# Performance work log

Measured on AMD Instinct MI355X. Metric: run time of the kernel, lower is better.

The kernel has to match this reference:

```python
import jax, jax.numpy as jnp
import numpy as np

B, S, K = 32, 256, 3   # batch, lattice length, max predecessors
D = 512                # dim_embedding == dim_rnn_input
H = 512                # dim_hidden
V = 50257              # vocab_size
L = 128                # label_vocab_size


def lattice_lstm(x, prev_idx, prev_w, Wih, Whh, bih, bhh):
    # x: [B,S,D]; prev_idx/prev_w: [B,S,K]; PyTorch LSTM gate layout (i,f,g,o).
    Bs, Sl, _ = x.shape
    Hh = Whh.shape[1]
    b_ar = jnp.arange(Bs)[:, None]  # [B,1] batch index for gather

    def step(carry, xs):
        hs, cs = carry              # stored per-timestep states [S,B,H]
        t, x_t, idx_t, w_t = xs     # [], [B,D], [B,K], [B,K]
        # weighted gather-pool over lattice predecessors; hs/cs are zero-init
        # so at t==0 this yields the zero initial state, as in the original.
        h = jnp.einsum('bk,bkh->bh', w_t, hs[idx_t, b_ar])
        c = jnp.einsum('bk,bkh->bh', w_t, cs[idx_t, b_ar])
        gates = x_t @ Wih.T + h @ Whh.T + (bih + bhh)  # [B,4H]
        i, f, g, o = jnp.split(gates, 4, axis=-1)
        c_new = jax.nn.sigmoid(f) * c + jax.nn.sigmoid(i) * jnp.tanh(g)
        h_new = jax.nn.sigmoid(o) * jnp.tanh(c_new)
        return (hs.at[t].set(h_new), cs.at[t].set(c_new)), h_new

    z = jnp.zeros((Sl, Bs, Hh), x.dtype)
    xs = (jnp.arange(Sl), x.swapaxes(0, 1), prev_idx.swapaxes(0, 1), prev_w.swapaxes(0, 1))
    _, outs = jax.lax.scan(step, (z, z), xs)
    return outs.swapaxes(0, 1)  # [B,S,H]


def _forward(inputs, positions, prev_idx, prev_w, emb, Wih, Whh, bih, bhh, W_lin, b_lin):
    x = emb[inputs]  # [B,S,D]
    out = lattice_lstm(x, prev_idx, prev_w, Wih, Whh, bih, bhh)
    # max-pool over the [start, end) span per batch element
    t_idx = jnp.arange(out.shape[1])[None, :]
    start, end = positions[:, 0:1], positions[:, 1:2]
    mask = (t_idx >= start) & (t_idx < end)                  # [B,S]
    pooled = jnp.where(mask[..., None], out, -1e30).max(axis=1)
    pooled = jnp.where(end > start, pooled, 0.0)             # empty span -> zeros
    return pooled @ W_lin.T + b_lin                          # [B,L]


def setup_inputs():
    key = jax.random.key(0)
    ks = jax.random.split(key, 12)
    inputs = jax.random.randint(ks[0], (B, S), 0, V)
    positions = jnp.concatenate([
        jax.random.randint(ks[1], (B, 1), 0, S // 2),
        jax.random.randint(ks[2], (B, 1), S // 2, S + 1)], axis=1)
    # predecessor indices must point strictly before t (DAG topological order)
    t = jnp.arange(S)[None, :, None]
    prev_idx = jax.random.randint(ks[3], (B, S, K), 0, S) % jnp.maximum(t, 1)
    u = jax.random.uniform(ks[4], (B, S, K)) + 0.1
    prev_w = u / u.sum(-1, keepdims=True)  # lattice marginals, sum to 1
    s = 1.0 / np.sqrt(H)
    emb = jax.random.uniform(ks[5], (V, D), minval=-0.1, maxval=0.1)
    Wih = jax.random.uniform(ks[6], (4 * H, D), minval=-s, maxval=s)
    Whh = jax.random.uniform(ks[7], (4 * H, H), minval=-s, maxval=s)
    bih = jax.random.uniform(ks[8], (4 * H,), minval=-s, maxval=s)
    bhh = jax.random.uniform(ks[9], (4 * H,), minval=-s, maxval=s)
    W_lin = jax.random.uniform(ks[10], (L, H), minval=-s, maxval=s)
    b_lin = jax.random.uniform(ks[11], (L,), minval=-s, maxval=s)
    return {"inputs": inputs, "positions": positions, "prev_idx": prev_idx,
            "prev_w": prev_w, "emb": emb, "Wih": Wih, "Whh": Whh,
            "bih": bih, "bhh": bhh, "W_lin": W_lin, "b_lin": b_lin}


def reference(inputs, positions, prev_idx, prev_w, emb, Wih, Whh, bih, bhh, W_lin, b_lin):
    return _forward(inputs, positions, prev_idx, prev_w, emb, Wih, Whh, bih, bhh, W_lin, b_lin)
```

## Files before the change

### kernel.cpp

```cpp
#include <hip/hip_runtime.h>


#define BB 32
#define SS 256
#define KKK 3
#define DD 512
#define HH 512
#define G4 2048
#define LL 128
#define NG 2
#define GS 8
#define NB 16
#define HSL 64

typedef __attribute__((ext_vector_type(4))) float f32x4;
typedef __attribute__((ext_vector_type(8))) short bf16x8;

__device__ __forceinline__ float blo(unsigned u){ return __builtin_bit_cast(float, u << 16); }
__device__ __forceinline__ float bhi(unsigned u){ return __builtin_bit_cast(float, u & 0xffff0000u); }
__device__ __forceinline__ unsigned f2bf(float f){
  unsigned x = __builtin_bit_cast(unsigned, f);
  x = x + 0x7fffu + ((x >> 16) & 1u);
  return x >> 16;
}
__device__ __forceinline__ float sigm(float x){ return 1.0f / (1.0f + __expf(-x)); }
__device__ __forceinline__ float tanh_(float x){
  float ax = fabsf(x);
  float e = __expf(-2.0f * ax);
  float r = (1.0f - e) / (1.0f + e);
  return x < 0.0f ? -r : r;
}
__device__ __forceinline__ void glds16(const void* g, void* lds){
  __builtin_amdgcn_global_load_lds((const __attribute__((address_space(1))) unsigned int*)g,
                                   (__attribute__((address_space(3))) unsigned int*)lds, 16, 0, 0);
}

__global__ __launch_bounds__(256) void prep_kernel(
    const int* __restrict__ inputs, const float* __restrict__ emb,
    const float* __restrict__ Wih, const float* __restrict__ bih, const float* __restrict__ bhh,
    unsigned short* __restrict__ Xb, unsigned short* __restrict__ Wihb, float* __restrict__ bias)
{
  int blk = blockIdx.x, tid = threadIdx.x;
  if (blk < 512){
    int row = blk * 16 + (tid >> 4);
    int d0 = (tid & 15) * 32;
    int b = row & 31, t = row >> 5;
    int tok = inputs[b * SS + t];
    const float* src = emb + (size_t)tok * DD + d0;
    unsigned short* dst = Xb + (size_t)row * DD + d0;
    #pragma unroll
    for (int j = 0; j < 32; j += 4){
      float4 v = *(const float4*)(src + j);
      uint2 o;
      o.x = f2bf(v.x) | (f2bf(v.y) << 16);
      o.y = f2bf(v.z) | (f2bf(v.w) << 16);
      *(uint2*)(dst + j) = o;
    }
  } else if (blk < 640){
    int row = (blk - 512) * 16 + (tid >> 4);
    int d0 = (tid & 15) * 32;
    const float* src = Wih + (size_t)row * DD + d0;
    unsigned short* dst = Wihb + (size_t)row * DD + d0;
    #pragma unroll
    for (int j = 0; j < 32; j += 4){
      float4 v = *(const float4*)(src + j);
      uint2 o;
      o.x = f2bf(v.x) | (f2bf(v.y) << 16);
      o.y = f2bf(v.z) | (f2bf(v.w) << 16);
      *(uint2*)(dst + j) = o;
    }
  } else {
    for (int n = tid; n < G4; n += 256) bias[n] = bih[n] + bhh[n];
  }
}

__global__ __launch_bounds__(256) void gemm_gx(
    const unsigned short* __restrict__ Xb, const unsigned short* __restrict__ Wihb,
    const float* __restrict__ bias, unsigned short* __restrict__ gx)
{
  __shared__ unsigned short As[128 * 32];
  __shared__ unsigned short Bs[128 * 32];
  const int tid = threadIdx.x;
  const int lane = tid & 63, wid = tid >> 6;
  const int m0 = blockIdx.x * 128, n0 = blockIdx.y * 128;
  const int wm = wid & 1, wn = wid >> 1;
  f32x4 acc[4][4];
  #pragma unroll
  for (int i = 0; i < 4; i++)
    #pragma unroll
    for (int j = 0; j < 4; j++)
      acc[i][j] = (f32x4){0.f, 0.f, 0.f, 0.f};

  for (int kk = 0; kk < DD; kk += 32){
    #pragma unroll
    for (int r = 0; r < 2; r++){
      int q = r * 256 + wid * 64 + lane;
      int row = q >> 2, seg = q & 3;
      glds16(Xb   + (size_t)(m0 + row) * DD + kk + seg * 8, As + (size_t)(r * 256 + wid * 64) * 8);
      glds16(Wihb + (size_t)(n0 + row) * DD + kk + seg * 8, Bs + (size_t)(r * 256 + wid * 64) * 8);
    }
    __syncthreads();
    bf16x8 af[4], bfv[4];
    #pragma unroll
    for (int i = 0; i < 4; i++){
      int ra = wm * 64 + i * 16 + (lane & 15);
      af[i] = *(const bf16x8*)(As + ra * 32 + (lane >> 4) * 8);
      int rb = wn * 64 + i * 16 + (lane & 15);
      bfv[i] = *(const bf16x8*)(Bs + rb * 32 + (lane >> 4) * 8);
    }
    #pragma unroll
    for (int i = 0; i < 4; i++)
      #pragma unroll
      for (int j = 0; j < 4; j++)
        acc[i][j] = __builtin_amdgcn_mfma_f32_16x16x32_bf16(af[i], bfv[j], acc[i][j], 0, 0, 0);
    __syncthreads();
  }
  #pragma unroll
  for (int j = 0; j < 4; j++){
    int ncol = n0 + wn * 64 + j * 16 + (lane & 15);
    float bv = bias[ncol];
    #pragma unroll
    for (int i = 0; i < 4; i++){
      int mbase = m0 + wm * 64 + i * 16 + (lane >> 4) * 4;
      #pragma unroll
      for (int r = 0; r < 4; r++)
        gx[(size_t)(mbase + r) * G4 + ncol] = (unsigned short)f2bf(acc[i][j][r] + bv);
    }
  }
}

__global__ __launch_bounds__(512, 1) void recur8(
    const int* __restrict__ prev_idx, const float* __restrict__ prev_w,
    const float* __restrict__ Whh, const int* __restrict__ positions,
    const unsigned short* __restrict__ gx,
    unsigned short* __restrict__ h_hist, float* __restrict__ c_hist,
    float* __restrict__ pooled, unsigned int* __restrict__ tags)
{
  __shared__ __align__(16) unsigned char hA[16 * 1024];
  __shared__ float gex[NB][264];
  __shared__ float wst2[2][NB * 3];
  __shared__ int   ist2[2][NB * 3];
  __shared__ int   wm_l[GS];
  __shared__ int   mneed2[2];
  __shared__ int   flag_s;

  const int tid = threadIdx.x;
  const int lane = tid & 63, w = tid >> 6;
  const int bid = blockIdx.x, grp = bid >> 3, g = bid & 7;

  bf16x8 bfr0[16], bfr1[16];
  #pragma unroll
  for (int kf = 0; kf < 16; kf++){
    #pragma unroll
    for (int i = 0; i < 2; i++){
      int nt = 2 * w + i;
      int grow = (nt >> 2) * HH + g * HSL + ((nt & 3) << 4) + (lane & 15);
      int kcol = kf * 32 + ((lane >> 4) << 3);
      const float* p = Whh + (size_t)grow * HH + kcol;
      float4 v0 = *(const float4*)p;
      float4 v1 = *(const float4*)(p + 4);
      bf16x8 tf;
      tf[0] = (short)f2bf(v0.x); tf[1] = (short)f2bf(v0.y);
      tf[2] = (short)f2bf(v0.z); tf[3] = (short)f2bf(v0.w);
      tf[4] = (short)f2bf(v1.x); tf[5] = (short)f2bf(v1.y);
      tf[6] = (short)f2bf(v1.z); tf[7] = (short)f2bf(v1.w);
      if (i == 0) bfr0[kf] = tf; else bfr1[kf] = tf;
    }
  }

  const int cb = tid >> 5;
  const int jd = (tid & 31) << 1;
  const int bg = grp * NB + cb;
  const int gq = tid & 15;
  const int gd = tid >> 4;
  const int ggs = gd >> 2;
  const int gdof = (gd & 3) << 4;

  const int st = positions[bg * 2], en = positions[bg * 2 + 1];
  float pm0 = -1e30f, pm1 = -1e30f;
  const size_t cblk = (size_t)bid * ((size_t)SS * NB * HSL);
  const unsigned long long* hq = (const unsigned long long*)h_hist;
  unsigned* hbw = (unsigned*)h_hist;

  unsigned long long dq0[4], dq1[4], dq2[4];
  float2 cg0, cg1, cg2;
  unsigned gxv0, gxv1, gxv2, gxv3;

  if (tid < GS) wm_l[tid] = 0;
  __syncthreads();

  auto issue_gather = [&](int slot){
    int i0 = ist2[slot][gq * 3], i1 = ist2[slot][gq * 3 + 1], i2 = ist2[slot][gq * 3 + 2];
    size_t s0 = (((((size_t)i0 * NG + grp) * GS + ggs) * NB + gq) * HSL + gdof) >> 2;
    size_t s1 = (((((size_t)i1 * NG + grp) * GS + ggs) * NB + gq) * HSL + gdof) >> 2;
    size_t s2 = (((((size_t)i2 * NG + grp) * GS + ggs) * NB + gq) * HSL + gdof) >> 2;
    #pragma unroll
    for (int j = 0; j < 4; j++)
      dq0[j] = __hip_atomic_load(hq + s0 + j, __ATOMIC_RELAXED, __HIP_MEMORY_SCOPE_AGENT);
    #pragma unroll
    for (int j = 0; j < 4; j++)
      dq1[j] = __hip_atomic_load(hq + s1 + j, __ATOMIC_RELAXED, __HIP_MEMORY_SCOPE_AGENT);
    #pragma unroll
    for (int j = 0; j < 4; j++)
      dq2[j] = __hip_atomic_load(hq + s2 + j, __ATOMIC_RELAXED, __HIP_MEMORY_SCOPE_AGENT);
  };
  auto issue_cgx = [&](int slot, int tn){
    const float* cb0 = c_hist + cblk + (size_t)cb * HSL + jd;
    cg0 = *(const float2*)(cb0 + (size_t)ist2[slot][cb * 3]     * (NB * HSL));
    cg1 = *(const float2*)(cb0 + (size_t)ist2[slot][cb * 3 + 1] * (NB * HSL));
    cg2 = *(const float2*)(cb0 + (size_t)ist2[slot][cb * 3 + 2] * (NB * HSL));
    const unsigned short* gxr = gx + ((size_t)tn * BB + bg) * G4 + g * HSL + jd;
    gxv0 = *(const unsigned*)(gxr);
    gxv1 = *(const unsigned*)(gxr + 512);
    gxv2 = *(const unsigned*)(gxr + 1024);
    gxv3 = *(const unsigned*)(gxr + 1536);
  };

  {
    const unsigned short* gxr = gx + (size_t)bg * G4 + g * HSL + jd;
    gxv0 = *(const unsigned*)(gxr);
    gxv1 = *(const unsigned*)(gxr + 512);
    gxv2 = *(const unsigned*)(gxr + 1024);
    gxv3 = *(const unsigned*)(gxr + 1536);
    int iv = -1;
    if (tid < NB * 3){
      int b = tid / 3, k = tid - b * 3;
      iv = prev_idx[(size_t)(grp * NB + b) * (SS * KKK) + 1 * KKK + k];
      ist2[1][tid] = iv;
      wst2[1][tid] = prev_w[(size_t)(grp * NB + b) * (SS * KKK) + 1 * KKK + k];
    }
    if (tid < 64){
      int m = iv;
      #pragma unroll
      for (int off = 32; off; off >>= 1) m = max(m, __shfl_xor(m, off));
      if (tid == 0) mneed2[1] = m;
    }
    float cn0 = sigm(blo(gxv0)) * tanh_(blo(gxv2));
    float cn1 = sigm(bhi(gxv0)) * tanh_(bhi(gxv2));
    float hn0 = sigm(blo(gxv3)) * tanh_(cn0);
    float hn1 = sigm(bhi(gxv3)) * tanh_(cn1);
    *(float2*)(c_hist + cblk + (size_t)cb * HSL + jd) = make_float2(cn0, cn1);
    unsigned hv = f2bf(hn0) | (f2bf(hn1) << 16);
    __hip_atomic_store(hbw + (((((size_t)grp * GS + g) * NB + cb) * HSL + jd) >> 1), hv,
                       __ATOMIC_RELAXED, __HIP_MEMORY_SCOPE_AGENT);
    if (0 >= st && 0 < en){ pm0 = fmaxf(pm0, hn0); pm1 = fmaxf(pm1, hn1); }
    __syncthreads();
    if (tid == 0){
      __hip_atomic_store(&tags[grp * GS + g], 1u, __ATOMIC_RELAXED, __HIP_MEMORY_SCOPE_AGENT);
      wm_l[g] = 1;
      int m = wm_l[0];
      #pragma unroll
      for (int p = 1; p < GS; p++) m = min(m, wm_l[p]);
      flag_s = (m >= mneed2[1] + 1) ? 1 : 0;
    }
    __syncthreads();
  }
  bool valid = (flag_s != 0);
  if (valid) issue_gather(1);
  issue_cgx(1, 1);

  for (int t = 1; t < SS; t++){
    const int sl = t & 1, sn = sl ^ 1;

    unsigned tsnap = 0;
    if (tid < GS)
      tsnap = __hip_atomic_load(&tags[grp * GS + tid], __ATOMIC_RELAXED,
                                __HIP_MEMORY_SCOPE_AGENT);

    if (!valid){
      const int need = mneed2[sl] + 1;
      if (tid < GS){
        int v = wm_l[tid];
        if (v < need){
          const unsigned int* tp = tags + grp * GS + tid;
          do {
            v = (int)__hip_atomic_load(tp, __ATOMIC_RELAXED, __HIP_MEMORY_SCOPE_AGENT);
            if (v < need) __builtin_amdgcn_s_sleep(1);
          } while (v < need);
          wm_l[tid] = v;
        }
      }
      __syncthreads();
      issue_gather(sl);
    }

    {
      float w0 = wst2[sl][gq * 3], w1 = wst2[sl][gq * 3 + 1], w2 = wst2[sl][gq * 3 + 2];
      unsigned pk[8];
      #pragma unroll
      for (int j = 0; j < 4; j++){
        unsigned a_lo = (unsigned)dq0[j], a_hi = (unsigned)(dq0[j] >> 32);
        unsigned b_lo = (unsigned)dq1[j], b_hi = (unsigned)(dq1[j] >> 32);
        unsigned c_lo = (unsigned)dq2[j], c_hi = (unsigned)(dq2[j] >> 32);
        float l0 = w0 * blo(a_lo) + w1 * blo(b_lo) + w2 * blo(c_lo);
        float h0 = w0 * bhi(a_lo) + w1 * bhi(b_lo) + w2 * bhi(c_lo);
        float l1 = w0 * blo(a_hi) + w1 * blo(b_hi) + w2 * blo(c_hi);
        float h1 = w0 * bhi(a_hi) + w1 * bhi(b_hi) + w2 * bhi(c_hi);
        pk[2 * j]     = f2bf(l0) | (f2bf(h0) << 16);
        pk[2 * j + 1] = f2bf(l1) | (f2bf(h1) << 16);
      }
      int ob = (gq << 10) + gd * 32;
      int xr = (gq & 7) << 4;
      *(uint4*)(hA + (ob ^ xr))        = (uint4){pk[0], pk[1], pk[2], pk[3]};
      *(uint4*)(hA + ((ob + 16) ^ xr)) = (uint4){pk[4], pk[5], pk[6], pk[7]};
    }
    __syncthreads();

    int iv = -1;
    if (t + 1 < SS){
      if (tid < NB * 3){
        int b = tid / 3, k = tid - b * 3;
        iv = prev_idx[(size_t)(grp * NB + b) * (SS * KKK) + (t + 1) * KKK + k];
        ist2[sn][tid] = iv;
        wst2[sn][tid] = prev_w[(size_t)(grp * NB + b) * (SS * KKK) + (t + 1) * KKK + k];
      }
    }
    {
      f32x4 p00 = {0,0,0,0}, p01 = {0,0,0,0}, p10 = {0,0,0,0}, p11 = {0,0,0,0};
      const int rA = lane & 15;
      const int kb = (lane >> 4) << 4;
      const int xr = (rA & 7) << 4;
      const int rbase = rA << 10;
      #pragma unroll
      for (int kf = 0; kf < 16; kf += 2){
        bf16x8 a0 = *(const bf16x8*)(hA + ((rbase + kf * 64 + kb) ^ xr));
        bf16x8 a1 = *(const bf16x8*)(hA + ((rbase + (kf + 1) * 64 + kb) ^ xr));
        p00 = __builtin_amdgcn_mfma_f32_16x16x32_bf16(a0, bfr0[kf],     p00, 0, 0, 0);
        p10 = __builtin_amdgcn_mfma_f32_16x16x32_bf16(a0, bfr1[kf],     p10, 0, 0, 0);
        p01 = __builtin_amdgcn_mfma_f32_16x16x32_bf16(a1, bfr0[kf + 1], p01, 0, 0, 0);
        p11 = __builtin_amdgcn_mfma_f32_16x16x32_bf16(a1, bfr1[kf + 1], p11, 0, 0, 0);
      }
      int cl0 = (2 * w) * 16 + rA, cl1 = cl0 + 16;
      #pragma unroll
      for (int j = 0; j < 4; j++){
        int bq = ((lane >> 4) << 2) + j;
        gex[bq][cl0] = p00[j] + p01[j];
        gex[bq][cl1] = p10[j] + p11[j];
      }
    }
    if (t + 1 < SS && tid < 64){
      int m = iv;
      #pragma unroll
      for (int off = 32; off; off >>= 1) m = max(m, __shfl_xor(m, off));
      if (tid == 0) mneed2[sn] = m;
    }
    __syncthreads();

    {
      float w0 = wst2[sl][cb * 3], w1 = wst2[sl][cb * 3 + 1], w2 = wst2[sl][cb * 3 + 2];
      float g_i0 = blo(gxv0) + gex[cb][jd];
      float g_i1 = bhi(gxv0) + gex[cb][jd + 1];
      float g_f0 = blo(gxv1) + gex[cb][64 + jd];
      float g_f1 = bhi(gxv1) + gex[cb][64 + jd + 1];
      float g_g0 = blo(gxv2) + gex[cb][128 + jd];
      float g_g1 = bhi(gxv2) + gex[cb][128 + jd + 1];
      float g_o0 = blo(gxv3) + gex[cb][192 + jd];
      float g_o1 = bhi(gxv3) + gex[cb][192 + jd + 1];
      float co0 = w0 * cg0.x + w1 * cg1.x + w2 * cg2.x;
      float co1 = w0 * cg0.y + w1 * cg1.y + w2 * cg2.y;
      float cn0 = sigm(g_f0) * co0 + sigm(g_i0) * tanh_(g_g0);
      float cn1 = sigm(g_f1) * co1 + sigm(g_i1) * tanh_(g_g1);
      float hn0 = sigm(g_o0) * tanh_(cn0);
      float hn1 = sigm(g_o1) * tanh_(cn1);
      *(float2*)(c_hist + cblk + ((size_t)t * NB + cb) * HSL + jd) = make_float2(cn0, cn1);
      unsigned hv = f2bf(hn0) | (f2bf(hn1) << 16);
      __hip_atomic_store(hbw + ((((((size_t)t * NG + grp) * GS + g) * NB + cb) * HSL + jd) >> 1),
                         hv, __ATOMIC_RELAXED, __HIP_MEMORY_SCOPE_AGENT);
      if (t >= st && t < en){ pm0 = fmaxf(pm0, hn0); pm1 = fmaxf(pm1, hn1); }
    }
    if (tid < GS) wm_l[tid] = max(wm_l[tid], (int)tsnap);
    __syncthreads();

    if (tid == 0){
      __hip_atomic_store(&tags[grp * GS + g], (unsigned)(t + 1),
                         __ATOMIC_RELAXED, __HIP_MEMORY_SCOPE_AGENT);
      wm_l[g] = t + 1;
      int f = 0;
      if (t + 1 < SS){
        int m = wm_l[0];
        #pragma unroll
        for (int p = 1; p < GS; p++) m = min(m, wm_l[p]);
        f = (m >= mneed2[sn] + 1) ? 1 : 0;
      }
      flag_s = f;
    }
    __syncthreads();
    valid = (flag_s != 0);
    if (t + 1 < SS){
      if (valid) issue_gather(sn);
      issue_cgx(sn, t + 1);
    }
  }

  pooled[(size_t)bg * HH + g * HSL + jd]     = (en > st && pm0 > -1e29f) ? pm0 : 0.f;
  pooled[(size_t)bg * HH + g * HSL + jd + 1] = (en > st && pm1 > -1e29f) ? pm1 : 0.f;
}

__global__ __launch_bounds__(128) void pool_lin(
    const float* __restrict__ pooled, const float* __restrict__ W_lin,
    const float* __restrict__ b_lin, float* __restrict__ out)
{
  __shared__ float p[HH];
  int b = blockIdx.x, tid = threadIdx.x;
  *(float4*)&p[tid * 4] = *(const float4*)&pooled[(size_t)b * HH + tid * 4];
  __syncthreads();
  float acc = b_lin[tid];
  const float* wr = W_lin + (size_t)tid * HH;
  #pragma unroll 8
  for (int h = 0; h < HH; h += 4){
    float4 w = *(const float4*)(wr + h);
    acc += w.x * p[h] + w.y * p[h+1] + w.z * p[h+2] + w.w * p[h+3];
  }
  out[b * LL + tid] = acc;
}

extern "C" void kernel_launch(void* const* d_in, const int* in_sizes, int n_in,
                              void* d_out, int out_size, void* d_ws, size_t ws_size,
                              hipStream_t stream)
{
  (void)in_sizes; (void)n_in; (void)out_size; (void)ws_size;
  const int*   inputs    = (const int*)  d_in[0];
  const int*   positions = (const int*)  d_in[1];
  const int*   prev_idx  = (const int*)  d_in[2];
  const float* prev_w    = (const float*)d_in[3];
  const float* emb       = (const float*)d_in[4];
  const float* Wih       = (const float*)d_in[5];
  const float* Whh       = (const float*)d_in[6];
  const float* bih       = (const float*)d_in[7];
  const float* bhh       = (const float*)d_in[8];
  const float* W_lin     = (const float*)d_in[9];
  const float* b_lin     = (const float*)d_in[10];
  float* out = (float*)d_out;
  char* ws = (char*)d_ws;

  unsigned int*   tags   = (unsigned int*)  ws;
  unsigned short* Xb     = (unsigned short*)(ws + 4096);
  unsigned short* Wihb   = (unsigned short*)(ws + 8392704);
  float*          bias   = (float*)         (ws + 10489856);
  unsigned short* gx     = (unsigned short*)(ws + 10498048);
  unsigned short* h_hist = (unsigned short*)(ws + 44052480);
  float*          c_hist = (float*)         (ws + 52441088);
  float*          pooled = (float*)         (ws + 69218304);

  hipMemsetAsync(tags, 0, 4096, stream);
  prep_kernel<<<641, 256, 0, stream>>>(inputs, emb, Wih, bih, bhh, Xb, Wihb, bias);
  gemm_gx<<<dim3(64, 16), 256, 0, stream>>>(Xb, Wihb, bias, gx);
  recur8<<<16, 512, 0, stream>>>(prev_idx, prev_w, Whh, positions, gx, h_hist, c_hist, pooled, tags);
  pool_lin<<<32, 128, 0, stream>>>(pooled, W_lin, b_lin, out);
}
```

Baseline: 1.476 ms.

## Decide next-step gather readiness earlier and drop a block barrier per step

The readiness check for the next timestep's predecessor-state gather now runs right after the recurrent MFMA phase, using the tag snapshot, instead of after the state update. Speculative gathers are therefore issued earlier and overlap the gate nonlinearities. The tid==0 flag computation and one __syncthreads per step go away, and the spin wait skips the block's own tag. It relies on subtler reasoning about memory visibility: the block's own freshly written h is never counted as ready early, so gathers that need it fall back to the spin-wait path.

```diff
diff --git a/kernel.cpp b/kernel.cpp
--- a/kernel.cpp
+++ b/kernel.cpp
@@ -129,7 +129,7 @@
   }
 }
 
-__global__ __launch_bounds__(512, 1) void recur8(
+__global__ __launch_bounds__(512, 1) void recur9(
     const int* __restrict__ prev_idx, const float* __restrict__ prev_w,
     const float* __restrict__ Whh, const int* __restrict__ positions,
     const unsigned short* __restrict__ gx,
@@ -141,8 +141,8 @@
   __shared__ float wst2[2][NB * 3];
   __shared__ int   ist2[2][NB * 3];
   __shared__ int   wm_l[GS];
+  __shared__ int   snap_l[GS];
   __shared__ int   mneed2[2];
-  __shared__ int   flag_s;
 
   const int tid = threadIdx.x;
   const int lane = tid & 63, w = tid >> 6;
@@ -186,7 +186,7 @@
   float2 cg0, cg1, cg2;
   unsigned gxv0, gxv1, gxv2, gxv3;
 
-  if (tid < GS) wm_l[tid] = 0;
+  if (tid < GS){ wm_l[tid] = 0; snap_l[tid] = 0; }
   __syncthreads();
 
   auto issue_gather = [&](int slot){
@@ -248,16 +248,10 @@
     if (tid == 0){
       __hip_atomic_store(&tags[grp * GS + g], 1u, __ATOMIC_RELAXED, __HIP_MEMORY_SCOPE_AGENT);
       wm_l[g] = 1;
-      int m = wm_l[0];
-      #pragma unroll
-      for (int p = 1; p < GS; p++) m = min(m, wm_l[p]);
-      flag_s = (m >= mneed2[1] + 1) ? 1 : 0;
-    }
-    __syncthreads();
-  }
-  bool valid = (flag_s != 0);
-  if (valid) issue_gather(1);
-  issue_cgx(1, 1);
+    }
+    issue_cgx(1, 1);
+  }
+  bool valid = false;
 
   for (int t = 1; t < SS; t++){
     const int sl = t & 1, sn = sl ^ 1;
@@ -269,7 +263,7 @@
 
     if (!valid){
       const int need = mneed2[sl] + 1;
-      if (tid < GS){
+      if (tid < GS && tid != g){
         int v = wm_l[tid];
         if (v < need){
           const unsigned int* tp = tags + grp * GS + tid;
@@ -344,7 +338,18 @@
       for (int off = 32; off; off >>= 1) m = max(m, __shfl_xor(m, off));
       if (tid == 0) mneed2[sn] = m;
     }
-    __syncthreads();
+    if (tid < GS) snap_l[tid] = (int)tsnap;
+    __syncthreads();
+
+    bool validn = false;
+    if (t + 1 < SS){
+      const int need = mneed2[sn] + 1;
+      int m = max(wm_l[0], snap_l[0]);
+      #pragma unroll
+      for (int p = 1; p < GS; p++) m = min(m, max(wm_l[p], snap_l[p]));
+      validn = (m >= need);
+      if (validn) issue_gather(sn);
+    }
 
     {
       float w0 = wst2[sl][cb * 3], w1 = wst2[sl][cb * 3 + 1], w2 = wst2[sl][cb * 3 + 2];
@@ -368,28 +373,15 @@
                          hv, __ATOMIC_RELAXED, __HIP_MEMORY_SCOPE_AGENT);
       if (t >= st && t < en){ pm0 = fmaxf(pm0, hn0); pm1 = fmaxf(pm1, hn1); }
     }
-    if (tid < GS) wm_l[tid] = max(wm_l[tid], (int)tsnap);
-    __syncthreads();
-
-    if (tid == 0){
+    if (tid < GS) wm_l[tid] = max(wm_l[tid], snap_l[tid]);
+    __syncthreads();
+
+    if (tid == 0)
       __hip_atomic_store(&tags[grp * GS + g], (unsigned)(t + 1),
                          __ATOMIC_RELAXED, __HIP_MEMORY_SCOPE_AGENT);
-      wm_l[g] = t + 1;
-      int f = 0;
-      if (t + 1 < SS){
-        int m = wm_l[0];
-        #pragma unroll
-        for (int p = 1; p < GS; p++) m = min(m, wm_l[p]);
-        f = (m >= mneed2[sn] + 1) ? 1 : 0;
-      }
-      flag_s = f;
-    }
-    __syncthreads();
-    valid = (flag_s != 0);
-    if (t + 1 < SS){
-      if (valid) issue_gather(sn);
+    if (t + 1 < SS)
       issue_cgx(sn, t + 1);
-    }
+    valid = validn;
   }
 
   pooled[(size_t)bg * HH + g * HSL + jd]     = (en > st && pm0 > -1e29f) ? pm0 : 0.f;
@@ -445,6 +437,6 @@
   hipMemsetAsync(tags, 0, 4096, stream);
   prep_kernel<<<641, 256, 0, stream>>>(inputs, emb, Wih, bih, bhh, Xb, Wihb, bias);
   gemm_gx<<<dim3(64, 16), 256, 0, stream>>>(Xb, Wihb, bias, gx);
-  recur8<<<16, 512, 0, stream>>>(prev_idx, prev_w, Whh, positions, gx, h_hist, c_hist, pooled, tags);
+  recur9<<<16, 512, 0, stream>>>(prev_idx, prev_w, Whh, positions, gx, h_hist, c_hist, pooled, tags);
   pool_lin<<<32, 128, 0, stream>>>(pooled, W_lin, b_lin, out);
 }
```

After: 1.455 ms (median of 2 runs). No clear change (-1.4%).
